# Optimization experiments

Measured on AMD Instinct MI355X. Metric: run time of the kernel, lower is better.

## Reference

```python
import jax, jax.numpy as jnp
import numpy as np

B, N, F_IN, F_OUT = 16, 1024, 128, 128

def setup_inputs() -> dict:
    key = jax.random.key(0)
    k1, k2, k3 = jax.random.split(key, 3)
    X = jax.random.normal(k1, (B, N, F_IN), dtype=jnp.float32)
    A = jax.random.uniform(k2, (B, N, N), dtype=jnp.float32)
    W = jax.random.normal(k3, (F_IN, F_OUT), dtype=jnp.float32)
    return {"X": X, "A": A, "W": W}

def reference(X, A, W):
    # A_hat = A + I  (batched add of identity)
    n = A.shape[-1]
    A_hat = A + jnp.eye(n, dtype=A.dtype)  # [B,N,N]
    # D_hat^{-1/2} applied as elementwise row/col scaling (torch builds diag
    # matrices and inverts; mathematically identical for diagonal D).
    deg = jnp.sum(A_hat, axis=-1)               # [B,N]
    d_inv_sqrt = 1.0 / jnp.sqrt(deg)            # [B,N]
    A_norm = A_hat * d_inv_sqrt[:, :, None] * d_inv_sqrt[:, None, :]  # [B,N,N]
    out = jnp.einsum('bnm,bmf->bnf', A_norm, X)  # aggregation bmm
    out = jnp.einsum('bnf,fg->bng', out, W)      # weight matmul
    return out
```

## Files before the change

kernel.cpp:

```cpp
#include <hip/hip_runtime.h>

#define NN 1024
#define FF 128

typedef __attribute__((ext_vector_type(8))) short bf16x8;
typedef __attribute__((ext_vector_type(4))) float f32x4;

__device__ __forceinline__ unsigned short f2bf(float x) {
  unsigned u = __float_as_uint(x);
  u += 0x7fff + ((u >> 16) & 1);
  return (unsigned short)(u >> 16);
}
__device__ __forceinline__ float bf2f(unsigned short b) {
  return __uint_as_float(((unsigned)b) << 16);
}
__device__ __forceinline__ bf16x8 cvt8(float4 a, float4 b) {
  bf16x8 r;
  r[0] = (short)f2bf(a.x); r[1] = (short)f2bf(a.y);
  r[2] = (short)f2bf(a.z); r[3] = (short)f2bf(a.w);
  r[4] = (short)f2bf(b.x); r[5] = (short)f2bf(b.y);
  r[6] = (short)f2bf(b.z); r[7] = (short)f2bf(b.w);
  return r;
}

__device__ __forceinline__ void gl_lds16(const void* g, void* l) {
  __builtin_amdgcn_global_load_lds(
      (const __attribute__((address_space(1))) unsigned*)g,
      (__attribute__((address_space(3))) unsigned*)l, 16, 0, 0);
}

__global__ __launch_bounds__(256) void k_deg(const float* __restrict__ A,
                                             const float* __restrict__ W,
                                             float* __restrict__ d,
                                             unsigned short* __restrict__ Wt,
                                             unsigned short* __restrict__ Abf) {
  if (blockIdx.x >= 4096) {
    int id = (blockIdx.x - 4096) * 256 + threadIdx.x;
    int g = id >> 7, f = id & 127;
    Wt[g * 128 + f] = f2bf(W[f * 128 + g]);
    return;
  }
  int row  = blockIdx.x * 4 + (threadIdx.x >> 6);
  int lane = threadIdx.x & 63;
  const float4* Ar = (const float4*)(A + (size_t)row * NN);
  unsigned short* Br = Abf + (size_t)row * NN;
  float s = 0.f;
#pragma unroll
  for (int i = 0; i < 4; ++i) {
    float4 v = Ar[lane + i * 64];
    ushort4 p; p.x = f2bf(v.x); p.y = f2bf(v.y); p.z = f2bf(v.z); p.w = f2bf(v.w);
    *(ushort4*)(Br + (lane + i * 64) * 4) = p;
    s += (v.x + v.y) + (v.z + v.w);
  }
#pragma unroll
  for (int off = 32; off > 0; off >>= 1) s += __shfl_down(s, off, 64);
  if (lane == 0) d[row] = rsqrtf(s + 1.0f);
}

__global__ __launch_bounds__(256) void k_xw(const float* __restrict__ X,
                                            const unsigned short* __restrict__ Wt,
                                            const float* __restrict__ d,
                                            unsigned short* __restrict__ Yt) {
  __shared__ __align__(16) unsigned short Xs[64 * 128];
  __shared__ __align__(16) unsigned short Ws[128 * 128];
  __shared__ float dl[64];
  int t  = threadIdx.x;
  int b  = blockIdx.x >> 4;
  int m0 = (blockIdx.x & 15) * 64;

#pragma unroll
  for (int j = 0; j < 4; ++j) {
    int id = t + j * 256;
    int r = id >> 4, p = id & 15, c = p ^ (r & 15);
    const float* gp = X + ((size_t)(b * NN + m0 + r) * FF + c * 8);
    float4 v0 = *(const float4*)gp;
    float4 v1 = *(const float4*)(gp + 4);
    *(bf16x8*)&Xs[r * 128 + p * 8] = cvt8(v0, v1);
  }
#pragma unroll
  for (int j = 0; j < 8; ++j) {
    int id = t + j * 256;
    int g = id >> 4, p = id & 15, c = p ^ (g & 15);
    uint4 v = *(const uint4*)(Wt + g * 128 + c * 8);
    *(uint4*)&Ws[g * 128 + p * 8] = v;
  }
  if (t < 64) dl[t] = d[b * NN + m0 + t];
  __syncthreads();

  int wave = t >> 6, lane = t & 63, quad = lane >> 4, l16 = lane & 15;
  f32x4 acc[8];
#pragma unroll
  for (int ct = 0; ct < 8; ++ct) acc[ct] = (f32x4){0.f, 0.f, 0.f, 0.f};

#pragma unroll
  for (int ks = 0; ks < 4; ++ks) {
    int q = ks * 4 + quad;
    bf16x8 a = *(const bf16x8*)&Xs[(wave * 16 + l16) * 128 + (q ^ l16) * 8];
#pragma unroll
    for (int ct = 0; ct < 8; ++ct) {
      bf16x8 w = *(const bf16x8*)&Ws[(ct * 16 + l16) * 128 + (q ^ l16) * 8];
      acc[ct] = __builtin_amdgcn_mfma_f32_16x16x32_bf16(a, w, acc[ct], 0, 0, 0);
    }
  }

  int mb = wave * 16 + quad * 4;
  float4 d4 = *(const float4*)&dl[mb];
#pragma unroll
  for (int ct = 0; ct < 8; ++ct) {
    int g = ct * 16 + l16;
    ushort4 p;
    p.x = f2bf(d4.x * acc[ct][0]);
    p.y = f2bf(d4.y * acc[ct][1]);
    p.z = f2bf(d4.z * acc[ct][2]);
    p.w = f2bf(d4.w * acc[ct][3]);
    *(ushort4*)(Yt + (size_t)(b * 128 + g) * NN + m0 + mb) = p;
  }
}

__global__ __launch_bounds__(256, 2) void k_agg(const unsigned short* __restrict__ Abf,
                                                const unsigned short* __restrict__ Yt,
                                                const float* __restrict__ d,
                                                float* __restrict__ out) {
  __shared__ __align__(16) unsigned short As[32 * 128];
  __shared__ __align__(16) unsigned short Ys[128 * 128];
  int t  = threadIdx.x;
  int b  = blockIdx.x >> 5;
  int n0 = (blockIdx.x & 31) * 32;
  int wave = t >> 6, lane = t & 63, quad = lane >> 4, l16 = lane & 15;
  int wr = wave >> 1, wc = wave & 1;
  int rl = lane >> 4, pl = lane & 15;

  const unsigned short* Ab = Abf + (size_t)(b * NN + n0) * NN;
  const unsigned short* Yb = Yt + (size_t)b * 128 * NN;

  auto issue = [&](int k0) {
#pragma unroll
    for (int j = 0; j < 2; ++j) {
      int r0 = wave * 8 + j * 4;
      int r  = r0 + rl;
      int c  = pl ^ (r & 15);
      gl_lds16(Ab + ((size_t)r * NN + k0 + c * 8), &As[r0 * 128]);
    }
#pragma unroll
    for (int j = 0; j < 8; ++j) {
      int r0 = wave * 32 + j * 4;
      int r  = r0 + rl;
      int c  = pl ^ (r & 15);
      gl_lds16(Yb + ((size_t)r * NN + k0 + c * 8), &Ys[r0 * 128]);
    }
  };

  f32x4 acc[4];
#pragma unroll
  for (int ct = 0; ct < 4; ++ct) acc[ct] = (f32x4){0.f, 0.f, 0.f, 0.f};

  issue(0);
  for (int s = 0; s < 8; ++s) {
    __syncthreads();
#pragma unroll
    for (int ks = 0; ks < 4; ++ks) {
      int cq = ks * 4 + quad;
      bf16x8 a = *(const bf16x8*)&As[(wr * 16 + l16) * 128 + (cq ^ l16) * 8];
#pragma unroll
      for (int ct = 0; ct < 4; ++ct) {
        bf16x8 y = *(const bf16x8*)&Ys[(wc * 64 + ct * 16 + l16) * 128 + (cq ^ l16) * 8];
        acc[ct] = __builtin_amdgcn_mfma_f32_16x16x32_bf16(a, y, acc[ct], 0, 0, 0);
      }
    }
    __syncthreads();
    if (s < 7) issue((s + 1) * 128);
  }

  int nb = n0 + wr * 16 + quad * 4;
  float4 d4 = *(const float4*)(d + b * NN + nb);
#pragma unroll
  for (int ct = 0; ct < 4; ++ct) {
    int g = wc * 64 + ct * 16 + l16;
    ushort4 yv = *(const ushort4*)(Yt + (size_t)(b * 128 + g) * NN + nb);
    float* op = out + ((size_t)(b * NN + nb) * FF + g);
    op[0 * FF] = d4.x * (acc[ct][0] + bf2f(yv.x));
    op[1 * FF] = d4.y * (acc[ct][1] + bf2f(yv.y));
    op[2 * FF] = d4.z * (acc[ct][2] + bf2f(yv.z));
    op[3 * FF] = d4.w * (acc[ct][3] + bf2f(yv.w));
  }
}

extern "C" void kernel_launch(void* const* d_in, const int* in_sizes, int n_in,
                              void* d_out, int out_size, void* d_ws, size_t ws_size,
                              hipStream_t stream) {
  const float* X = (const float*)d_in[0];
  const float* A = (const float*)d_in[1];
  const float* W = (const float*)d_in[2];
  float* out = (float*)d_out;

  char* ws = (char*)d_ws;
  float*          dinv = (float*)ws;
  unsigned short* Wt   = (unsigned short*)(ws + 65536);
  unsigned short* Yt   = (unsigned short*)(ws + 98304);
  unsigned short* Abf  = (unsigned short*)(ws + 98304 + 4194304);

  k_deg<<<dim3(4096 + 64), dim3(256), 0, stream>>>(A, W, dinv, Wt, Abf);
  k_xw <<<dim3(256),       dim3(256), 0, stream>>>(X, Wt, dinv, Yt);
  k_agg<<<dim3(512),       dim3(256), 0, stream>>>(Abf, Yt, dinv, out);
}
```

Measured before the change: 120.1 us.

## Fuse degree/A-conversion into XW kernel; double-buffer and XCD-remap aggregation

```diff
diff --git a/kernel.cpp b/kernel.cpp
--- a/kernel.cpp
+++ b/kernel.cpp
@@ -29,44 +29,67 @@
       (__attribute__((address_space(3))) unsigned*)l, 16, 0, 0);
 }
 
-__global__ __launch_bounds__(256) void k_deg(const float* __restrict__ A,
-                                             const float* __restrict__ W,
+__global__ __launch_bounds__(256) void k_wt(const float* __restrict__ W,
+                                            unsigned short* __restrict__ Wt) {
+  int id = blockIdx.x * 256 + threadIdx.x;
+  int g = id >> 7, f = id & 127;
+  Wt[g * 128 + f] = f2bf(W[f * 128 + g]);
+}
+
+__global__ __launch_bounds__(256) void k_pre(const float* __restrict__ A,
+                                             const float* __restrict__ X,
+                                             const unsigned short* __restrict__ Wt,
                                              float* __restrict__ d,
-                                             unsigned short* __restrict__ Wt,
-                                             unsigned short* __restrict__ Abf) {
-  if (blockIdx.x >= 4096) {
-    int id = (blockIdx.x - 4096) * 256 + threadIdx.x;
-    int g = id >> 7, f = id & 127;
-    Wt[g * 128 + f] = f2bf(W[f * 128 + g]);
-    return;
-  }
-  int row  = blockIdx.x * 4 + (threadIdx.x >> 6);
-  int lane = threadIdx.x & 63;
-  const float4* Ar = (const float4*)(A + (size_t)row * NN);
-  unsigned short* Br = Abf + (size_t)row * NN;
-  float s = 0.f;
-#pragma unroll
-  for (int i = 0; i < 4; ++i) {
-    float4 v = Ar[lane + i * 64];
-    ushort4 p; p.x = f2bf(v.x); p.y = f2bf(v.y); p.z = f2bf(v.z); p.w = f2bf(v.w);
-    *(ushort4*)(Br + (lane + i * 64) * 4) = p;
-    s += (v.x + v.y) + (v.z + v.w);
-  }
-#pragma unroll
-  for (int off = 32; off > 0; off >>= 1) s += __shfl_down(s, off, 64);
-  if (lane == 0) d[row] = rsqrtf(s + 1.0f);
-}
-
-__global__ __launch_bounds__(256) void k_xw(const float* __restrict__ X,
-                                            const unsigned short* __restrict__ Wt,
-                                            const float* __restrict__ d,
-                                            unsigned short* __restrict__ Yt) {
+                                             unsigned short* __restrict__ Abf,
+                                             unsigned short* __restrict__ Yt) {
   __shared__ __align__(16) unsigned short Xs[64 * 128];
   __shared__ __align__(16) unsigned short Ws[128 * 128];
   __shared__ float dl[64];
   int t  = threadIdx.x;
   int b  = blockIdx.x >> 4;
   int m0 = (blockIdx.x & 15) * 64;
+  int wave = t >> 6, lane = t & 63;
+
+  {
+    float rs[16];
+#pragma unroll
+    for (int i0 = 0; i0 < 16; i0 += 4) {
+      float4 v[4][4];
+#pragma unroll
+      for (int i = 0; i < 4; ++i) {
+        size_t grow = (size_t)b * NN + m0 + wave * 16 + i0 + i;
+        const float4* Ar = (const float4*)(A + grow * NN);
+#pragma unroll
+        for (int k = 0; k < 4; ++k) v[i][k] = Ar[lane + k * 64];
+      }
+#pragma unroll
+      for (int i = 0; i < 4; ++i) {
+        size_t grow = (size_t)b * NN + m0 + wave * 16 + i0 + i;
+        unsigned short* Br = Abf + grow * NN;
+        float s = 0.f;
+#pragma unroll
+        for (int k = 0; k < 4; ++k) {
+          float4 w = v[i][k];
+          ushort4 p; p.x = f2bf(w.x); p.y = f2bf(w.y); p.z = f2bf(w.z); p.w = f2bf(w.w);
+          *(ushort4*)(Br + (lane + k * 64) * 4) = p;
+          s += (w.x + w.y) + (w.z + w.w);
+        }
+        rs[i0 + i] = s;
+      }
+    }
+#pragma unroll
+    for (int i = 0; i < 16; ++i) {
+      float s = rs[i];
+#pragma unroll
+      for (int off = 32; off > 0; off >>= 1) s += __shfl_down(s, off, 64);
+      if (lane == 0) {
+        float dv = rsqrtf(s + 1.0f);
+        int r = wave * 16 + i;
+        dl[r] = dv;
+        d[(size_t)b * NN + m0 + r] = dv;
+      }
+    }
+  }
 
 #pragma unroll
   for (int j = 0; j < 4; ++j) {
@@ -84,10 +107,9 @@
     uint4 v = *(const uint4*)(Wt + g * 128 + c * 8);
     *(uint4*)&Ws[g * 128 + p * 8] = v;
   }
-  if (t < 64) dl[t] = d[b * NN + m0 + t];
   __syncthreads();
 
-  int wave = t >> 6, lane = t & 63, quad = lane >> 4, l16 = lane & 15;
+  int quad = lane >> 4, l16 = lane & 15;
   f32x4 acc[8];
 #pragma unroll
   for (int ct = 0; ct < 8; ++ct) acc[ct] = (f32x4){0.f, 0.f, 0.f, 0.f};
@@ -121,11 +143,14 @@
                                                 const unsigned short* __restrict__ Yt,
                                                 const float* __restrict__ d,
                                                 float* __restrict__ out) {
-  __shared__ __align__(16) unsigned short As[32 * 128];
-  __shared__ __align__(16) unsigned short Ys[128 * 128];
-  int t  = threadIdx.x;
-  int b  = blockIdx.x >> 5;
-  int n0 = (blockIdx.x & 31) * 32;
+  __shared__ __align__(16) unsigned short As[2][32 * 128];
+  __shared__ __align__(16) unsigned short Ys[2][128 * 128];
+  int t   = threadIdx.x;
+  int bid = blockIdx.x;
+  int xcd = bid & 7;
+  int j   = bid >> 3;
+  int b   = xcd + 8 * (j >> 5);
+  int n0  = (j & 31) * 32;
   int wave = t >> 6, lane = t & 63, quad = lane >> 4, l16 = lane & 15;
   int wr = wave >> 1, wc = wave & 1;
   int rl = lane >> 4, pl = lane & 15;
@@ -133,20 +158,20 @@
   const unsigned short* Ab = Abf + (size_t)(b * NN + n0) * NN;
   const unsigned short* Yb = Yt + (size_t)b * 128 * NN;
 
-  auto issue = [&](int k0) {
-#pragma unroll
-    for (int j = 0; j < 2; ++j) {
-      int r0 = wave * 8 + j * 4;
+  auto issue = [&](int k0, int buf) {
+#pragma unroll
+    for (int jj = 0; jj < 2; ++jj) {
+      int r0 = wave * 8 + jj * 4;
       int r  = r0 + rl;
       int c  = pl ^ (r & 15);
-      gl_lds16(Ab + ((size_t)r * NN + k0 + c * 8), &As[r0 * 128]);
-    }
-#pragma unroll
-    for (int j = 0; j < 8; ++j) {
-      int r0 = wave * 32 + j * 4;
+      gl_lds16(Ab + ((size_t)r * NN + k0 + c * 8), &As[buf][r0 * 128]);
+    }
+#pragma unroll
+    for (int jj = 0; jj < 8; ++jj) {
+      int r0 = wave * 32 + jj * 4;
       int r  = r0 + rl;
       int c  = pl ^ (r & 15);
-      gl_lds16(Yb + ((size_t)r * NN + k0 + c * 8), &Ys[r0 * 128]);
+      gl_lds16(Yb + ((size_t)r * NN + k0 + c * 8), &Ys[buf][r0 * 128]);
     }
   };
 
@@ -154,21 +179,21 @@
 #pragma unroll
   for (int ct = 0; ct < 4; ++ct) acc[ct] = (f32x4){0.f, 0.f, 0.f, 0.f};
 
-  issue(0);
+  issue(0, 0);
   for (int s = 0; s < 8; ++s) {
+    int cur = s & 1;
     __syncthreads();
+    if (s < 7) issue((s + 1) * 128, cur ^ 1);
 #pragma unroll
     for (int ks = 0; ks < 4; ++ks) {
       int cq = ks * 4 + quad;
-      bf16x8 a = *(const bf16x8*)&As[(wr * 16 + l16) * 128 + (cq ^ l16) * 8];
+      bf16x8 a = *(const bf16x8*)&As[cur][(wr * 16 + l16) * 128 + (cq ^ l16) * 8];
 #pragma unroll
       for (int ct = 0; ct < 4; ++ct) {
-        bf16x8 y = *(const bf16x8*)&Ys[(wc * 64 + ct * 16 + l16) * 128 + (cq ^ l16) * 8];
+        bf16x8 y = *(const bf16x8*)&Ys[cur][(wc * 64 + ct * 16 + l16) * 128 + (cq ^ l16) * 8];
         acc[ct] = __builtin_amdgcn_mfma_f32_16x16x32_bf16(a, y, acc[ct], 0, 0, 0);
       }
     }
-    __syncthreads();
-    if (s < 7) issue((s + 1) * 128);
   }
 
   int nb = n0 + wr * 16 + quad * 4;
@@ -199,7 +224,7 @@
   unsigned short* Yt   = (unsigned short*)(ws + 98304);
   unsigned short* Abf  = (unsigned short*)(ws + 98304 + 4194304);
 
-  k_deg<<<dim3(4096 + 64), dim3(256), 0, stream>>>(A, W, dinv, Wt, Abf);
-  k_xw <<<dim3(256),       dim3(256), 0, stream>>>(X, Wt, dinv, Yt);
-  k_agg<<<dim3(512),       dim3(256), 0, stream>>>(Abf, Yt, dinv, out);
-}
+  k_wt <<<dim3(64),  dim3(256), 0, stream>>>(W, Wt);
+  k_pre<<<dim3(256), dim3(256), 0, stream>>>(A, X, Wt, dinv, Abf, Yt);
+  k_agg<<<dim3(512), dim3(256), 0, stream>>>(Abf, Yt, dinv, out);
+}
```

Result: slower. 130.6 us (+8.7%).

## Drop bf16 copy of A; load fp32 A directly in aggregation and convert in-register

Applied to the files above, without the earlier changes.

```diff
diff --git a/kernel.cpp b/kernel.cpp
--- a/kernel.cpp
+++ b/kernel.cpp
@@ -32,8 +32,7 @@
 __global__ __launch_bounds__(256) void k_deg(const float* __restrict__ A,
                                              const float* __restrict__ W,
                                              float* __restrict__ d,
-                                             unsigned short* __restrict__ Wt,
-                                             unsigned short* __restrict__ Abf) {
+                                             unsigned short* __restrict__ Wt) {
   if (blockIdx.x >= 4096) {
     int id = (blockIdx.x - 4096) * 256 + threadIdx.x;
     int g = id >> 7, f = id & 127;
@@ -43,13 +42,10 @@
   int row  = blockIdx.x * 4 + (threadIdx.x >> 6);
   int lane = threadIdx.x & 63;
   const float4* Ar = (const float4*)(A + (size_t)row * NN);
-  unsigned short* Br = Abf + (size_t)row * NN;
   float s = 0.f;
 #pragma unroll
   for (int i = 0; i < 4; ++i) {
     float4 v = Ar[lane + i * 64];
-    ushort4 p; p.x = f2bf(v.x); p.y = f2bf(v.y); p.z = f2bf(v.z); p.w = f2bf(v.w);
-    *(ushort4*)(Br + (lane + i * 64) * 4) = p;
     s += (v.x + v.y) + (v.z + v.w);
   }
 #pragma unroll
@@ -117,11 +113,11 @@
   }
 }
 
-__global__ __launch_bounds__(256, 2) void k_agg(const unsigned short* __restrict__ Abf,
-                                                const unsigned short* __restrict__ Yt,
-                                                const float* __restrict__ d,
-                                                float* __restrict__ out) {
-  __shared__ __align__(16) unsigned short As[32 * 128];
+__global__ __launch_bounds__(256) void k_agg(const float* __restrict__ A,
+                                             const unsigned short* __restrict__ Yt,
+                                             const float* __restrict__ d,
+                                             float* __restrict__ out) {
+  __shared__ __align__(16) float          Asf[32 * 128];
   __shared__ __align__(16) unsigned short Ys[128 * 128];
   int t  = threadIdx.x;
   int b  = blockIdx.x >> 5;
@@ -129,21 +125,22 @@
   int wave = t >> 6, lane = t & 63, quad = lane >> 4, l16 = lane & 15;
   int wr = wave >> 1, wc = wave & 1;
   int rl = lane >> 4, pl = lane & 15;
-
-  const unsigned short* Ab = Abf + (size_t)(b * NN + n0) * NN;
+  int rh = lane >> 5, cc = lane & 31;
+
+  const float*          Ab = A  + (size_t)(b * NN + n0) * NN;
   const unsigned short* Yb = Yt + (size_t)b * 128 * NN;
 
   auto issue = [&](int k0) {
 #pragma unroll
-    for (int j = 0; j < 2; ++j) {
-      int r0 = wave * 8 + j * 4;
-      int r  = r0 + rl;
-      int c  = pl ^ (r & 15);
-      gl_lds16(Ab + ((size_t)r * NN + k0 + c * 8), &As[r0 * 128]);
-    }
-#pragma unroll
-    for (int j = 0; j < 8; ++j) {
-      int r0 = wave * 32 + j * 4;
+    for (int jj = 0; jj < 4; ++jj) {
+      int r0 = wave * 8 + jj * 2;
+      int r  = r0 + rh;
+      int c  = cc ^ (2 * (r & 15));
+      gl_lds16(Ab + ((size_t)r * NN + k0 + c * 4), &Asf[r0 * 128]);
+    }
+#pragma unroll
+    for (int jj = 0; jj < 8; ++jj) {
+      int r0 = wave * 32 + jj * 4;
       int r  = r0 + rl;
       int c  = pl ^ (r & 15);
       gl_lds16(Yb + ((size_t)r * NN + k0 + c * 8), &Ys[r0 * 128]);
@@ -154,16 +151,20 @@
 #pragma unroll
   for (int ct = 0; ct < 4; ++ct) acc[ct] = (f32x4){0.f, 0.f, 0.f, 0.f};
 
+  int swA = 2 * l16;
   issue(0);
   for (int s = 0; s < 8; ++s) {
     __syncthreads();
 #pragma unroll
     for (int ks = 0; ks < 4; ++ks) {
       int cq = ks * 4 + quad;
-      bf16x8 a = *(const bf16x8*)&As[(wr * 16 + l16) * 128 + (cq ^ l16) * 8];
+      int pa = (2 * cq) ^ swA;
+      float4 a0 = *(const float4*)&Asf[(wr * 16 + l16) * 128 + pa * 4];
+      float4 a1 = *(const float4*)&Asf[(wr * 16 + l16) * 128 + pa * 4 + 4];
+      bf16x8 a = cvt8(a0, a1);
 #pragma unroll
       for (int ct = 0; ct < 4; ++ct) {
-        bf16x8 y = *(const bf16x8*)&Ys[(wc * 64 + ct * 16 + l16) * 128 + (cq ^ l16) * 8];
+        bf16x8 y = *(const bf16x8*)&Ys[(wc * 64 + ct * 16 + l16) * 128 + ((cq ^ l16)) * 8];
         acc[ct] = __builtin_amdgcn_mfma_f32_16x16x32_bf16(a, y, acc[ct], 0, 0, 0);
       }
     }
@@ -197,9 +198,8 @@
   float*          dinv = (float*)ws;
   unsigned short* Wt   = (unsigned short*)(ws + 65536);
   unsigned short* Yt   = (unsigned short*)(ws + 98304);
-  unsigned short* Abf  = (unsigned short*)(ws + 98304 + 4194304);
-
-  k_deg<<<dim3(4096 + 64), dim3(256), 0, stream>>>(A, W, dinv, Wt, Abf);
+
+  k_deg<<<dim3(4096 + 64), dim3(256), 0, stream>>>(A, W, dinv, Wt);
   k_xw <<<dim3(256),       dim3(256), 0, stream>>>(X, Wt, dinv, Yt);
-  k_agg<<<dim3(512),       dim3(256), 0, stream>>>(Abf, Yt, dinv, out);
-}
+  k_agg<<<dim3(512),       dim3(256), 0, stream>>>(A, Yt, dinv, out);
+}
```

After: 121.8 us. About the same (+1.4%).

## Double-buffer LDS tiles in aggregation kernel and remap blocks per XCD

Applied to the files above, without the earlier changes.

```diff
diff --git a/kernel.cpp b/kernel.cpp
--- a/kernel.cpp
+++ b/kernel.cpp
@@ -117,15 +117,18 @@
   }
 }
 
-__global__ __launch_bounds__(256, 2) void k_agg(const unsigned short* __restrict__ Abf,
-                                                const unsigned short* __restrict__ Yt,
-                                                const float* __restrict__ d,
-                                                float* __restrict__ out) {
-  __shared__ __align__(16) unsigned short As[32 * 128];
-  __shared__ __align__(16) unsigned short Ys[128 * 128];
-  int t  = threadIdx.x;
-  int b  = blockIdx.x >> 5;
-  int n0 = (blockIdx.x & 31) * 32;
+__global__ __launch_bounds__(256) void k_agg(const unsigned short* __restrict__ Abf,
+                                             const unsigned short* __restrict__ Yt,
+                                             const float* __restrict__ d,
+                                             float* __restrict__ out) {
+  __shared__ __align__(16) unsigned short As[2][32 * 128];
+  __shared__ __align__(16) unsigned short Ys[2][128 * 128];
+  int t   = threadIdx.x;
+  int bid = blockIdx.x;
+  int xcd = bid & 7;
+  int j   = bid >> 3;
+  int b   = xcd + 8 * (j >> 5);
+  int n0  = (j & 31) * 32;
   int wave = t >> 6, lane = t & 63, quad = lane >> 4, l16 = lane & 15;
   int wr = wave >> 1, wc = wave & 1;
   int rl = lane >> 4, pl = lane & 15;
@@ -133,20 +136,20 @@
   const unsigned short* Ab = Abf + (size_t)(b * NN + n0) * NN;
   const unsigned short* Yb = Yt + (size_t)b * 128 * NN;
 
-  auto issue = [&](int k0) {
-#pragma unroll
-    for (int j = 0; j < 2; ++j) {
-      int r0 = wave * 8 + j * 4;
+  auto issue = [&](int k0, int buf) {
+#pragma unroll
+    for (int jj = 0; jj < 2; ++jj) {
+      int r0 = wave * 8 + jj * 4;
       int r  = r0 + rl;
       int c  = pl ^ (r & 15);
-      gl_lds16(Ab + ((size_t)r * NN + k0 + c * 8), &As[r0 * 128]);
-    }
-#pragma unroll
-    for (int j = 0; j < 8; ++j) {
-      int r0 = wave * 32 + j * 4;
+      gl_lds16(Ab + ((size_t)r * NN + k0 + c * 8), &As[buf][r0 * 128]);
+    }
+#pragma unroll
+    for (int jj = 0; jj < 8; ++jj) {
+      int r0 = wave * 32 + jj * 4;
       int r  = r0 + rl;
       int c  = pl ^ (r & 15);
-      gl_lds16(Yb + ((size_t)r * NN + k0 + c * 8), &Ys[r0 * 128]);
+      gl_lds16(Yb + ((size_t)r * NN + k0 + c * 8), &Ys[buf][r0 * 128]);
     }
   };
 
@@ -154,21 +157,21 @@
 #pragma unroll
   for (int ct = 0; ct < 4; ++ct) acc[ct] = (f32x4){0.f, 0.f, 0.f, 0.f};
 
-  issue(0);
+  issue(0, 0);
   for (int s = 0; s < 8; ++s) {
+    int cur = s & 1;
     __syncthreads();
+    if (s < 7) issue((s + 1) * 128, cur ^ 1);
 #pragma unroll
     for (int ks = 0; ks < 4; ++ks) {
       int cq = ks * 4 + quad;
-      bf16x8 a = *(const bf16x8*)&As[(wr * 16 + l16) * 128 + (cq ^ l16) * 8];
+      bf16x8 a = *(const bf16x8*)&As[cur][(wr * 16 + l16) * 128 + (cq ^ l16) * 8];
 #pragma unroll
       for (int ct = 0; ct < 4; ++ct) {
-        bf16x8 y = *(const bf16x8*)&Ys[(wc * 64 + ct * 16 + l16) * 128 + (cq ^ l16) * 8];
+        bf16x8 y = *(const bf16x8*)&Ys[cur][(wc * 64 + ct * 16 + l16) * 128 + (cq ^ l16) * 8];
         acc[ct] = __builtin_amdgcn_mfma_f32_16x16x32_bf16(a, y, acc[ct], 0, 0, 0);
       }
     }
-    __syncthreads();
-    if (s < 7) issue((s + 1) * 128);
   }
 
   int nb = n0 + wr * 16 + quad * 4;
```

Result: slower. 125.2 us (+4.2%).
